# Performance work log

Measured on AMD Instinct MI355X. Metric: run time of the kernel, lower is better.

## Reference

```python
import jax, jax.numpy as jnp
import numpy as np

N = 10000        # nodes
E = 160000       # edges (avg degree 16)
WIDTH = 32       # node hidden width
KER_W = 256      # kernel MLP hidden width
KER_IN = 6       # edge feature dim
DEPTH = 4        # message-passing iterations


def setup_inputs() -> dict:
    key = jax.random.key(0)
    ks = jax.random.split(key, 12)
    def w(k, shape, fan_in):
        return jax.random.normal(k, shape, jnp.float32) * (1.0 / np.sqrt(fan_in)).astype(np.float32)
    return {
        "x": jax.random.normal(ks[0], (N, 1), jnp.float32),
        "edge_index": jax.random.randint(ks[1], (2, E), 0, N),
        "edge_attr": jax.random.uniform(ks[2], (E, KER_IN), dtype=jnp.float32),
        # fc1: Linear(1, WIDTH)
        "fc1_w": w(ks[3], (1, WIDTH), 1), "fc1_b": jnp.zeros((WIDTH,), jnp.float32),
        # kernel DenseNet: KER_IN -> KER_W -> KER_W -> WIDTH^2 (ReLU between, none after last)
        "k1_w": w(ks[4], (KER_IN, KER_W), KER_IN), "k1_b": jnp.zeros((KER_W,), jnp.float32),
        "k2_w": w(ks[5], (KER_W, KER_W), KER_W), "k2_b": jnp.zeros((KER_W,), jnp.float32),
        "k3_w": w(ks[6], (KER_W, WIDTH * WIDTH), KER_W), "k3_b": jnp.zeros((WIDTH * WIDTH,), jnp.float32),
        # NNConv root weight + bias
        "root_w": w(ks[7], (WIDTH, WIDTH), WIDTH), "conv_b": jnp.zeros((WIDTH,), jnp.float32),
        # fc2: Linear(WIDTH, 1)
        "fc2_w": w(ks[8], (WIDTH, 1), WIDTH), "fc2_b": jnp.zeros((1,), jnp.float32),
    }


def reference(x, edge_index, edge_attr, fc1_w, fc1_b, k1_w, k1_b, k2_w, k2_b,
              k3_w, k3_b, root_w, conv_b, fc2_w, fc2_b):
    src, dst = edge_index[0], edge_index[1]  # messages flow src -> dst

    # Per-edge kernel weights (edge_attr is constant across depth -> compute once).
    h = jax.nn.relu(edge_attr @ k1_w + k1_b)
    h = jax.nn.relu(h @ k2_w + k2_b)
    W_e = (h @ k3_w + k3_b).reshape(E, WIDTH, WIDTH)  # [E, in, out]

    # Degree for scatter-mean (avoid div by zero).
    deg = jax.ops.segment_sum(jnp.ones((E,), jnp.float32), dst, num_segments=N)
    inv_deg = (1.0 / jnp.maximum(deg, 1.0))[:, None]

    h_node = x @ fc1_w + fc1_b  # [N, WIDTH]
    for _ in range(DEPTH):
        msg = jnp.einsum('ei,eio->eo', h_node[src], W_e)              # gather + per-edge GEMM
        agg = jax.ops.segment_sum(msg, dst, num_segments=N) * inv_deg  # scatter-mean
        h_node = jax.nn.relu(agg + h_node @ root_w + conv_b)
    return h_node @ fc2_w + fc2_b  # [N, 1]
```

## Files before the change

kernel.cpp:

```cpp
#include <hip/hip_runtime.h>
#include <hip/hip_fp16.h>

#define NNODE 10000
#define NEDGE 160000
#define W32 32
#define BSTR 40
#define PANEL_F16 10240
#define PANEL3_F16 5120
#define UB_TILES 20000

typedef _Float16 f16;
typedef _Float16 f16x4 __attribute__((ext_vector_type(4)));
typedef _Float16 f16x8 __attribute__((ext_vector_type(8)));
typedef float f32x4 __attribute__((ext_vector_type(4)));

__device__ __forceinline__ void stage_panel(f16* lds, const f16* g, int w, int lane) {
    #pragma unroll
    for (int i = 0; i < 5; ++i) {
        int slot = w * 320 + i * 64 + lane;
        __builtin_amdgcn_global_load_lds(
            (const __attribute__((address_space(1))) unsigned int*)(g + (size_t)slot * 8),
            (__attribute__((address_space(3))) unsigned int*)(lds + (size_t)(w * 320 + i * 64) * 8),
            16, 0, 0);
    }
}

__device__ __forceinline__ void stage_panel10k(f16* lds, const f16* g, int w, int lane) {
    #pragma unroll
    for (int i = 0; i < 2; ++i) {
        int base = i * 256 + w * 64;
        __builtin_amdgcn_global_load_lds(
            (const __attribute__((address_space(1))) unsigned int*)(g + (size_t)(base + lane) * 8),
            (__attribute__((address_space(3))) unsigned int*)(lds + (size_t)base * 8),
            16, 0, 0);
    }
    if (w < 2) {
        int base = 512 + w * 64;
        __builtin_amdgcn_global_load_lds(
            (const __attribute__((address_space(1))) unsigned int*)(g + (size_t)(base + lane) * 8),
            (__attribute__((address_space(3))) unsigned int*)(lds + (size_t)base * 8),
            16, 0, 0);
    }
}

__global__ __launch_bounds__(256) void pack_k1(const float* __restrict__ k1w, f16* __restrict__ k1p) {
    int t = blockIdx.x * 256 + threadIdx.x;
    int j = t / BSTR, c = t % BSTR;
    k1p[t] = (c < 6) ? (f16)k1w[c * 256 + j] : (f16)0.f;
}
__global__ __launch_bounds__(256) void pack_k2(const float* __restrict__ k2w, f16* __restrict__ k2p) {
    int t = blockIdx.x * 256 + threadIdx.x;
    int kk = t / PANEL_F16, r = t % PANEL_F16;
    int j = r / BSTR, c = r % BSTR;
    k2p[t] = (c < 32) ? (f16)k2w[(size_t)(kk * 32 + c) * 256 + j] : (f16)0.f;
}
__global__ __launch_bounds__(256) void pack_k3(const float* __restrict__ k3w, f16* __restrict__ k3p) {
    int t = blockIdx.x * 256 + threadIdx.x;
    int p = t / PANEL3_F16, r = t % PANEL3_F16;
    int np = p >> 3, kk = p & 7;
    int j = r / BSTR, c = r % BSTR;
    k3p[t] = (c < 32) ? (f16)k3w[(size_t)(kk * 32 + c) * 1024 + np * 128 + j] : (f16)0.f;
}
__global__ __launch_bounds__(256) void pack_k3t(const float* __restrict__ k3w, f16* __restrict__ k3t) {
    int t = blockIdx.x * 256 + threadIdx.x;
    int q = t / BSTR, i = t % BSTR;
    int o = q >> 8, c = q & 255;
    k3t[t] = (i < 32) ? (f16)k3w[(size_t)c * 1024 + i * 32 + o] : (f16)0.f;
}

__global__ __launch_bounds__(256) void h2_kernel(
    const float* __restrict__ ea,
    const f16* __restrict__ k1p, const float* __restrict__ k1b,
    const f16* __restrict__ k2p, const float* __restrict__ k2b,
    f16* __restrict__ h2c, int e_start, const int* __restrict__ remap)
{
    __shared__ __align__(16) f16 bls[2][256 * BSTR];
    __shared__ __align__(16) f16 ea_s[64 * BSTR];
    __shared__ __align__(16) f16 hbuf[64 * 264];

    const int t = threadIdx.x, w = t >> 6, lane = t & 63, quad = lane >> 4, l15 = lane & 15;
    const int el0 = blockIdx.x * 64;
    const int e0 = e_start + el0;

    stage_panel(bls[0], k1p, w, lane);
    for (int i = t; i < 64 * BSTR; i += 256) {
        int e = i / BSTR, c = i % BSTR;
        ea_s[i] = (f16)((c < 6) ? ea[(size_t)(e0 + e) * 6 + c] : 0.f);
    }
    __syncthreads();

    f16x8 a1 = *(const f16x8*)&ea_s[(w * 16 + l15) * BSTR + quad * 8];
    f32x4 acc[16];
    #pragma unroll
    for (int nt = 0; nt < 16; ++nt) { float b = k1b[nt * 16 + l15]; acc[nt] = (f32x4){b, b, b, b}; }
    stage_panel(bls[1], k2p, w, lane);
    #pragma unroll
    for (int nt = 0; nt < 16; ++nt) {
        f16x8 bf = *(const f16x8*)&bls[0][(nt * 16 + l15) * BSTR + quad * 8];
        acc[nt] = __builtin_amdgcn_mfma_f32_16x16x32_f16(a1, bf, acc[nt], 0, 0, 0);
    }
    #pragma unroll
    for (int nt = 0; nt < 16; ++nt)
        #pragma unroll
        for (int r = 0; r < 4; ++r)
            hbuf[(w * 16 + quad * 4 + r) * 264 + nt * 16 + l15] = (f16)fmaxf(acc[nt][r], 0.f);
    __syncthreads();

    f16x8 a2[8];
    #pragma unroll
    for (int kk = 0; kk < 8; ++kk)
        a2[kk] = *(const f16x8*)&hbuf[(w * 16 + l15) * 264 + kk * 32 + quad * 8];
    #pragma unroll
    for (int nt = 0; nt < 16; ++nt) { float b = k2b[nt * 16 + l15]; acc[nt] = (f32x4){b, b, b, b}; }
    for (int kk = 0; kk < 8; ++kk) {
        if (kk < 7)
            stage_panel(bls[kk & 1], k2p + (size_t)(kk + 1) * PANEL_F16, w, lane);
        const f16* B = bls[(kk + 1) & 1];
        #pragma unroll
        for (int nt = 0; nt < 16; ++nt) {
            f16x8 bf = *(const f16x8*)&B[(nt * 16 + l15) * BSTR + quad * 8];
            acc[nt] = __builtin_amdgcn_mfma_f32_16x16x32_f16(a2[kk], bf, acc[nt], 0, 0, 0);
        }
        __syncthreads();
    }
    size_t orow[4];
    #pragma unroll
    for (int r = 0; r < 4; ++r) {
        int eoff = w * 16 + quad * 4 + r;
        orow[r] = remap ? (size_t)remap[e0 + eoff] : (size_t)(el0 + eoff);
    }
    #pragma unroll
    for (int nt = 0; nt < 16; ++nt)
        #pragma unroll
        for (int r = 0; r < 4; ++r)
            h2c[orow[r] * 256 + nt * 16 + l15] = (f16)fmaxf(acc[nt][r], 0.f);
}

__global__ __launch_bounds__(256) void hist_kernel(const int* __restrict__ ei, int* __restrict__ cnt) {
    int e = blockIdx.x * 256 + threadIdx.x;
    if (e < NEDGE) atomicAdd(&cnt[ei[e]], 1);
}
__global__ __launch_bounds__(256) void scan_kernel(
    const int* __restrict__ cnt, int* __restrict__ edgeStart,
    int* __restrict__ tileStartN, int* __restrict__ cursor)
{
    __shared__ int pE[256], pT[256];
    const int t = threadIdx.x;
    int se = 0, st = 0;
    for (int k = 0; k < 40; ++k) {
        int n = t * 40 + k;
        if (n < NNODE) { int c = cnt[n]; se += c; st += (c + 15) >> 4; }
    }
    pE[t] = se; pT[t] = st;
    __syncthreads();
    if (t == 0) {
        int aE = 0, aT = 0;
        for (int i = 0; i < 256; ++i) { int tE = pE[i], tT = pT[i]; pE[i] = aE; pT[i] = aT; aE += tE; aT += tT; }
        tileStartN[NNODE] = aT;
    }
    __syncthreads();
    int oE = pE[t], oT = pT[t];
    for (int k = 0; k < 40; ++k) {
        int n = t * 40 + k;
        if (n < NNODE) {
            edgeStart[n] = oE; cursor[n] = oE; tileStartN[n] = oT;
            int c = cnt[n]; oE += c; oT += (c + 15) >> 4;
        }
    }
}
__global__ __launch_bounds__(256) void scatter_kernel(
    const int* __restrict__ ei, int* __restrict__ cursor,
    int* __restrict__ dstS, int* __restrict__ sortpos)
{
    int e = blockIdx.x * 256 + threadIdx.x;
    if (e < NEDGE) {
        int s = ei[e];
        int p = atomicAdd(&cursor[s], 1);
        dstS[p] = ei[NEDGE + e];
        sortpos[e] = p;
    }
}
__global__ __launch_bounds__(256) void tiles_kernel(
    const int* __restrict__ cnt, const int* __restrict__ edgeStart, const int* __restrict__ tileStartN,
    int* __restrict__ tileNode, int* __restrict__ tileE0, int* __restrict__ tileCnt)
{
    int n = blockIdx.x * 256 + threadIdx.x;
    if (n < NNODE) {
        int d = cnt[n], t0 = tileStartN[n], e0 = edgeStart[n];
        for (int k = 0; k * 16 < d; ++k) {
            int rem = d - k * 16;
            tileNode[t0 + k] = n;
            tileE0[t0 + k] = e0 + k * 16;
            tileCnt[t0 + k] = rem < 16 ? rem : 16;
        }
    }
}

__global__ __launch_bounds__(256) void bb_kernel(
    const float* __restrict__ h, const float* __restrict__ k3b, float* __restrict__ Bb)
{
    int idx = blockIdx.x * 256 + threadIdx.x;
    int n = idx >> 5, o = idx & 31;
    float s = 0.f;
    #pragma unroll
    for (int i = 0; i < 32; ++i)
        s += h[n * 32 + i] * k3b[i * 32 + o];
    Bb[idx] = s;
}

__global__ __launch_bounds__(256) void tgen_kernel(
    const float* __restrict__ h, const f16* __restrict__ k3t, f16* __restrict__ Tt,
    int n0, int n1)
{
    const int t = threadIdx.x, w = t >> 6, lane = t & 63, quad = lane >> 4, l15 = lane & 15;
    const int nBase = n0 + blockIdx.x * 16;
    const int colBase = blockIdx.y * 1024 + w * 256;

    f16x8 a;
    #pragma unroll
    for (int i = 0; i < 8; ++i) a[i] = (f16)0.f;
    int node = nBase + l15;
    if (node < n1) {
        const float4* hp = (const float4*)(h + (size_t)node * 32) + quad * 2;
        float4 v0 = hp[0], v1 = hp[1];
        a[0] = (f16)v0.x; a[1] = (f16)v0.y; a[2] = (f16)v0.z; a[3] = (f16)v0.w;
        a[4] = (f16)v1.x; a[5] = (f16)v1.y; a[6] = (f16)v1.z; a[7] = (f16)v1.w;
    }
    f32x4 acc[16];
    #pragma unroll
    for (int nt = 0; nt < 16; ++nt) {
        f16x8 bf = *(const f16x8*)&k3t[(size_t)(colBase + nt * 16 + l15) * BSTR + quad * 8];
        acc[nt] = __builtin_amdgcn_mfma_f32_16x16x32_f16(a, bf, (f32x4){0.f, 0.f, 0.f, 0.f}, 0, 0, 0);
    }
    #pragma unroll
    for (int r = 0; r < 4; ++r) {
        int nd = nBase + quad * 4 + r;
        if (nd < n1) {
            f16* dp = Tt + (size_t)(nd - n0) * 8192 + colBase + l15;
            #pragma unroll
            for (int nt = 0; nt < 16; ++nt)
                dp[nt * 16] = (f16)acc[nt][r];
        }
    }
}

__global__ __launch_bounds__(256) void msgT_kernel(
    const f16* __restrict__ h2s, const f16* __restrict__ Tt, const float* __restrict__ Bb,
    const int* __restrict__ tileNode, const int* __restrict__ tileE0, const int* __restrict__ tileCnt,
    const int* __restrict__ tileStartN, const int* __restrict__ dstS, float* __restrict__ agg,
    int n0, int n1)
{
    const int t = threadIdx.x, w = t >> 6, lane = t & 63, quad = lane >> 4, l15 = lane & 15;
    const int t0 = tileStartN[n0], t1 = tileStartN[n1];
    for (int tile = t0 + blockIdx.x * 4 + w; tile < t1; tile += gridDim.x * 4) {
        int n = tileNode[tile];
        int e0 = tileE0[tile], cnt = tileCnt[tile];
        const f16* Tn = Tt + (size_t)(n - n0) * 8192;
        f32x4 acc[2];
        #pragma unroll
        for (int nt = 0; nt < 2; ++nt) {
            float b = Bb[n * 32 + nt * 16 + l15];
            acc[nt] = (f32x4){b, b, b, b};
        }
        #pragma unroll
        for (int kk = 0; kk < 8; ++kk) {
            f16x8 a;
            #pragma unroll
            for (int i = 0; i < 8; ++i) a[i] = (f16)0.f;
            if (l15 < cnt)
                a = *(const f16x8*)&h2s[(size_t)(e0 + l15) * 256 + kk * 32 + quad * 8];
            #pragma unroll
            for (int nt = 0; nt < 2; ++nt) {
                f16x8 bf = *(const f16x8*)&Tn[(nt * 16 + l15) * 256 + kk * 32 + quad * 8];
                acc[nt] = __builtin_amdgcn_mfma_f32_16x16x32_f16(a, bf, acc[nt], 0, 0, 0);
            }
        }
        #pragma unroll
        for (int nt = 0; nt < 2; ++nt)
            #pragma unroll
            for (int r = 0; r < 4; ++r) {
                int er = quad * 4 + r;
                if (er < cnt)
                    atomicAdd(&agg[(size_t)dstS[e0 + er] * 32 + nt * 16 + l15], acc[nt][r]);
            }
    }
}

__global__ __launch_bounds__(256, 2) void msg_fused(
    const int* __restrict__ ei, const f16* __restrict__ h2c,
    const f16* __restrict__ k3p, const float* __restrict__ k3b,
    const float* __restrict__ h, float* __restrict__ agg, int e_start)
{
    __shared__ __align__(16) f16 bls[2][PANEL3_F16];
    __shared__ __align__(16) f16 h_s[256 * 36];
    __shared__ int dst_s[256];

    const int t = threadIdx.x, w = t >> 6, lane = t & 63, quad = lane >> 4, l15 = lane & 15;
    const int el0 = blockIdx.x * 256;
    const int e0 = e_start + el0;

    dst_s[t] = ei[NEDGE + e0 + t];
    {
        int srcn = ei[e0 + t];
        const float4* hr = (const float4*)(h + (size_t)srcn * 32);
        f16* dp = &h_s[t * 36];
        #pragma unroll
        for (int qq = 0; qq < 8; ++qq) {
            float4 v = hr[qq];
            dp[qq * 4 + 0] = (f16)v.x; dp[qq * 4 + 1] = (f16)v.y;
            dp[qq * 4 + 2] = (f16)v.z; dp[qq * 4 + 3] = (f16)v.w;
        }
    }
    stage_panel10k(bls[0], k3p, w, lane);

    float msg[4][4][2];
    #pragma unroll
    for (int m = 0; m < 4; ++m)
        #pragma unroll
        for (int r = 0; r < 4; ++r) { msg[m][r][0] = 0.f; msg[m][r][1] = 0.f; }

    f32x4 acc[4][8];
    __syncthreads();

    for (int it = 0; it < 64; ++it) {
        const int np = it >> 3, kk = it & 7;
        if (it) __syncthreads();
        if (it < 63) stage_panel10k(bls[(it + 1) & 1], k3p + (size_t)(it + 1) * PANEL3_F16, w, lane);

        f16x8 a[4];
        #pragma unroll
        for (int m = 0; m < 4; ++m)
            a[m] = *(const f16x8*)(h2c + (size_t)(el0 + w * 64 + m * 16 + l15) * 256 + kk * 32 + quad * 8);

        if (kk == 0) {
            #pragma unroll
            for (int nt = 0; nt < 8; ++nt) {
                float b = k3b[np * 128 + nt * 16 + l15];
                #pragma unroll
                for (int m = 0; m < 4; ++m) acc[m][nt] = (f32x4){b, b, b, b};
            }
        }
        const f16* B = bls[it & 1];
        #pragma unroll
        for (int nt = 0; nt < 8; ++nt) {
            f16x8 bf = *(const f16x8*)&B[(nt * 16 + l15) * BSTR + quad * 8];
            #pragma unroll
            for (int m = 0; m < 4; ++m)
                acc[m][nt] = __builtin_amdgcn_mfma_f32_16x16x32_f16(a[m], bf, acc[m][nt], 0, 0, 0);
        }
        if (kk == 7) {
            #pragma unroll
            for (int m = 0; m < 4; ++m)
                #pragma unroll
                for (int r = 0; r < 4; ++r) {
                    int row = w * 64 + m * 16 + quad * 4 + r;
                    f16x4 h4 = *(const f16x4*)&h_s[row * 36 + np * 4];
                    #pragma unroll
                    for (int nt = 0; nt < 8; ++nt)
                        msg[m][r][nt & 1] += (float)h4[nt >> 1] * acc[m][nt][r];
                }
        }
    }
    #pragma unroll
    for (int m = 0; m < 4; ++m)
        #pragma unroll
        for (int r = 0; r < 4; ++r) {
            int d = dst_s[w * 64 + m * 16 + quad * 4 + r];
            atomicAdd(&agg[d * W32 + l15],      msg[m][r][0]);
            atomicAdd(&agg[d * W32 + 16 + l15], msg[m][r][1]);
        }
}

__global__ __launch_bounds__(256) void h0_kernel(
    const float* __restrict__ x, const float* __restrict__ fc1w,
    const float* __restrict__ fc1b, float* __restrict__ h)
{
    int idx = blockIdx.x * 256 + threadIdx.x;
    int n = idx >> 5, j = idx & 31;
    h[idx] = x[n] * fc1w[j] + fc1b[j];
}

__global__ __launch_bounds__(256) void deg_kernel(
    const int* __restrict__ ei, float* __restrict__ deg)
{
    int e = blockIdx.x * 256 + threadIdx.x;
    if (e < NEDGE) atomicAdd(&deg[ei[NEDGE + e]], 1.f);
}

__global__ __launch_bounds__(256) void update_kernel(
    const float* __restrict__ h_old, float* __restrict__ h_new,
    float* __restrict__ agg, const float* __restrict__ deg,
    const float* __restrict__ rootw, const float* __restrict__ convb)
{
    __shared__ float rw[W32][W32 + 1];
    const int t = threadIdx.x;
    for (int q = t; q < W32 * W32; q += 256)
        rw[q >> 5][q & 31] = rootw[q];
    __syncthreads();
    const int nl = t >> 5, j = t & 31;
    const int n = blockIdx.x * 8 + nl;
    float hv = h_old[n * W32 + j];
    float acc = convb[j];
    #pragma unroll
    for (int k = 0; k < W32; ++k)
        acc += __shfl(hv, k, 32) * rw[k][j];
    float inv = 1.f / fmaxf(deg[n], 1.f);
    int idx = n * W32 + j;
    float a = agg[idx];
    agg[idx] = 0.f;
    h_new[idx] = fmaxf(a * inv + acc, 0.f);
}

__global__ __launch_bounds__(256) void out_kernel(
    const float* __restrict__ h, const float* __restrict__ fc2w,
    const float* __restrict__ fc2b, float* __restrict__ out)
{
    int n = blockIdx.x * 256 + threadIdx.x;
    if (n < NNODE) {
        float a = fc2b[0];
        #pragma unroll
        for (int j = 0; j < W32; ++j)
            a += h[n * W32 + j] * fc2w[j];
        out[n] = a;
    }
}

static inline size_t pad256(size_t x) { return (x + 255) & ~(size_t)255; }

extern "C" void kernel_launch(void* const* d_in, const int* in_sizes, int n_in,
                              void* d_out, int out_size, void* d_ws, size_t ws_size,
                              hipStream_t stream) {
    const float* x    = (const float*)d_in[0];
    const int*   ei   = (const int*)  d_in[1];
    const float* ea   = (const float*)d_in[2];
    const float* fc1w = (const float*)d_in[3];
    const float* fc1b = (const float*)d_in[4];
    const float* k1w  = (const float*)d_in[5];
    const float* k1b  = (const float*)d_in[6];
    const float* k2w  = (const float*)d_in[7];
    const float* k2b  = (const float*)d_in[8];
    const float* k3w  = (const float*)d_in[9];
    const float* k3b  = (const float*)d_in[10];
    const float* rootw= (const float*)d_in[11];
    const float* convb= (const float*)d_in[12];
    const float* fc2w = (const float*)d_in[13];
    const float* fc2b = (const float*)d_in[14];
    float* out = (float*)d_out;

    const size_t hbytes = (size_t)NNODE * W32 * 4;
    char* ws = (char*)d_ws;
    size_t off = 0;
    float* hA  = (float*)(ws + off); off += hbytes;
    float* hB  = (float*)(ws + off); off += hbytes;
    float* agg = (float*)(ws + off); off += hbytes;
    float* deg = (float*)(ws + off); off += 40960;
    f16*  k1p  = (f16*)(ws + off);   off += 20480;
    f16*  k2p  = (f16*)(ws + off);   off += 163840;
    f16*  k3p  = (f16*)(ws + off);   off += 655360;
    const size_t fixed = off;

    size_t toff = fixed;
    f16*  k3t      = (f16*)(ws + toff);  toff += pad256(8192 * BSTR * 2);
    int*  dstS     = (int*)(ws + toff);  toff += pad256((size_t)NEDGE * 4);
    int*  sortpos  = (int*)(ws + toff);  toff += pad256((size_t)NEDGE * 4);
    int*  cnt      = (int*)(ws + toff);  toff += pad256((size_t)NNODE * 4);
    int*  edgeStart= (int*)(ws + toff);  toff += pad256((size_t)NNODE * 4);
    int*  tileStartN=(int*)(ws + toff);  toff += pad256((size_t)(NNODE + 1) * 4);
    int*  cursor   = (int*)(ws + toff);  toff += pad256((size_t)NNODE * 4);
    int*  tileNode = (int*)(ws + toff);  toff += pad256((size_t)UB_TILES * 4);
    int*  tileE0   = (int*)(ws + toff);  toff += pad256((size_t)UB_TILES * 4);
    int*  tileCnt  = (int*)(ws + toff);  toff += pad256((size_t)UB_TILES * 4);
    float* Bb      = (float*)(ws + toff); toff += pad256((size_t)NNODE * 32 * 4);
    f16*  h2s      = (f16*)(ws + toff);  toff += pad256((size_t)NEDGE * 256 * 2);
    f16*  Tt       = (f16*)(ws + toff);

    int nc = 0, CS = 0;
    {
        const int cands[3] = {2, 4, 8};
        for (int ci = 0; ci < 3; ++ci) {
            int c = cands[ci];
            int cs = ((NNODE + c - 1) / c + 15) & ~15;
            size_t tb = (size_t)cs * 8192 * 2;
            if (ws_size >= toff + tb) { nc = c; CS = cs; break; }
        }
    }

    hipMemsetAsync(deg, 0, (size_t)NNODE * 4, stream);
    hipMemsetAsync(agg, 0, (size_t)NNODE * W32 * 4, stream);

    pack_k1<<<40, 256, 0, stream>>>(k1w, k1p);
    pack_k2<<<320, 256, 0, stream>>>(k2w, k2p);

    h0_kernel<<<NNODE * W32 / 256, 256, 0, stream>>>(x, fc1w, fc1b, hA);
    deg_kernel<<<(NEDGE + 255) / 256, 256, 0, stream>>>(ei, deg);

    float* hcur = hA; float* hnext = hB;

    if (nc) {
        pack_k3t<<<1280, 256, 0, stream>>>(k3w, k3t);
        hipMemsetAsync(cnt, 0, (size_t)NNODE * 4, stream);
        hist_kernel<<<(NEDGE + 255) / 256, 256, 0, stream>>>(ei, cnt);
        scan_kernel<<<1, 256, 0, stream>>>(cnt, edgeStart, tileStartN, cursor);
        scatter_kernel<<<(NEDGE + 255) / 256, 256, 0, stream>>>(ei, cursor, dstS, sortpos);
        tiles_kernel<<<(NNODE + 255) / 256, 256, 0, stream>>>(cnt, edgeStart, tileStartN,
                                                              tileNode, tileE0, tileCnt);
        h2_kernel<<<NEDGE / 64, 256, 0, stream>>>(ea, k1p, k1b, k2p, k2b, h2s, 0, sortpos);

        for (int d = 0; d < 4; ++d) {
            bb_kernel<<<NNODE * 32 / 256, 256, 0, stream>>>(hcur, k3b, Bb);
            for (int ct = 0; ct < nc; ++ct) {
                int n0 = ct * CS;
                if (n0 >= NNODE) break;
                int n1 = n0 + CS; if (n1 > NNODE) n1 = NNODE;
                dim3 tg((n1 - n0 + 15) / 16, 8);
                tgen_kernel<<<tg, 256, 0, stream>>>(hcur, k3t, Tt, n0, n1);
                msgT_kernel<<<1280, 256, 0, stream>>>(h2s, Tt, Bb, tileNode, tileE0, tileCnt,
                                                      tileStartN, dstS, agg, n0, n1);
            }
            update_kernel<<<NNODE / 8, 256, 0, stream>>>(hcur, hnext, agg, deg, rootw, convb);
            float* tmp = hcur; hcur = hnext; hnext = tmp;
        }
    } else {
        f16* h2b = (f16*)(ws + fixed);
        pack_k3<<<1280, 256, 0, stream>>>(k3w, k3p);

        long long availC = 0;
        if (ws_size > fixed) availC = (long long)((ws_size - fixed) / 512);
        int C = (availC > NEDGE) ? NEDGE : (int)availC;
        C &= ~255;
        if (C < 256) return;

        const bool full = (C == NEDGE);
        if (full)
            h2_kernel<<<NEDGE / 64, 256, 0, stream>>>(ea, k1p, k1b, k2p, k2b, h2b, 0, nullptr);

        for (int d = 0; d < 4; ++d) {
            for (int es = 0; es < NEDGE; es += C) {
                int ce = (NEDGE - es < C) ? (NEDGE - es) : C;
                if (!full)
                    h2_kernel<<<ce / 64, 256, 0, stream>>>(ea, k1p, k1b, k2p, k2b, h2b, es, nullptr);
                msg_fused<<<ce / 256, 256, 0, stream>>>(ei, h2b, k3p, k3b, hcur, agg, es);
            }
            update_kernel<<<NNODE / 8, 256, 0, stream>>>(hcur, hnext, agg, deg, rootw, convb);
            float* tmp = hcur; hcur = hnext; hnext = tmp;
        }
    }
    out_kernel<<<(NNODE + 255) / 256, 256, 0, stream>>>(hcur, fc2w, fc2b, out);
}
```

Baseline: 688.1 us.

## Stage MFMA outputs through LDS for coalesced 16-byte stores; allow single-chunk T buffer

In h2_kernel and tgen_kernel, MFMA results are first written to a padded LDS tile and then copied to global memory as contiguous 16-byte vectors per row. Previously each lane issued scattered 2-byte stores. The hbuf row stride is also changed to reduce LDS bank conflicts. Chunk count 1 is added to the candidate list, so the whole Tt buffer can be built in one pass when the workspace is large enough, cutting per-chunk launches. The cost is extra LDS traffic and barriers, plus a larger workspace requirement when one chunk is chosen.

```diff
diff --git a/kernel.cpp b/kernel.cpp
--- a/kernel.cpp
+++ b/kernel.cpp
@@ -8,6 +8,8 @@
 #define PANEL_F16 10240
 #define PANEL3_F16 5120
 #define UB_TILES 20000
+#define HB_STR 268
+#define TB_STR 1036
 
 typedef _Float16 f16;
 typedef _Float16 f16x4 __attribute__((ext_vector_type(4)));
@@ -76,7 +78,7 @@
 {
     __shared__ __align__(16) f16 bls[2][256 * BSTR];
     __shared__ __align__(16) f16 ea_s[64 * BSTR];
-    __shared__ __align__(16) f16 hbuf[64 * 264];
+    __shared__ __align__(16) f16 hbuf[64 * HB_STR];
 
     const int t = threadIdx.x, w = t >> 6, lane = t & 63, quad = lane >> 4, l15 = lane & 15;
     const int el0 = blockIdx.x * 64;
@@ -103,13 +105,13 @@
     for (int nt = 0; nt < 16; ++nt)
         #pragma unroll
         for (int r = 0; r < 4; ++r)
-            hbuf[(w * 16 + quad * 4 + r) * 264 + nt * 16 + l15] = (f16)fmaxf(acc[nt][r], 0.f);
+            hbuf[(w * 16 + quad * 4 + r) * HB_STR + nt * 16 + l15] = (f16)fmaxf(acc[nt][r], 0.f);
     __syncthreads();
 
     f16x8 a2[8];
     #pragma unroll
     for (int kk = 0; kk < 8; ++kk)
-        a2[kk] = *(const f16x8*)&hbuf[(w * 16 + l15) * 264 + kk * 32 + quad * 8];
+        a2[kk] = *(const f16x8*)&hbuf[(w * 16 + l15) * HB_STR + kk * 32 + quad * 8];
     #pragma unroll
     for (int nt = 0; nt < 16; ++nt) { float b = k2b[nt * 16 + l15]; acc[nt] = (f32x4){b, b, b, b}; }
     for (int kk = 0; kk < 8; ++kk) {
@@ -123,17 +125,23 @@
         }
         __syncthreads();
     }
-    size_t orow[4];
-    #pragma unroll
-    for (int r = 0; r < 4; ++r) {
-        int eoff = w * 16 + quad * 4 + r;
-        orow[r] = remap ? (size_t)remap[e0 + eoff] : (size_t)(el0 + eoff);
-    }
     #pragma unroll
     for (int nt = 0; nt < 16; ++nt)
         #pragma unroll
         for (int r = 0; r < 4; ++r)
-            h2c[orow[r] * 256 + nt * 16 + l15] = (f16)fmaxf(acc[nt][r], 0.f);
+            hbuf[(w * 16 + quad * 4 + r) * HB_STR + nt * 16 + l15] = (f16)fmaxf(acc[nt][r], 0.f);
+    __syncthreads();
+    {
+        const int row = t >> 2, u = t & 3;
+        const size_t orow = remap ? (size_t)remap[e0 + row] : (size_t)(el0 + row);
+        f16* gdst = h2c + orow * 256;
+        const f16* lsrc = &hbuf[row * HB_STR];
+        #pragma unroll
+        for (int j = 0; j < 8; ++j) {
+            int p = u + 4 * j;
+            *(f16x8*)(gdst + p * 8) = *(const f16x8*)(lsrc + p * 8);
+        }
+    }
 }
 
 __global__ __launch_bounds__(256) void hist_kernel(const int* __restrict__ ei, int* __restrict__ cnt) {
@@ -212,9 +220,11 @@
     const float* __restrict__ h, const f16* __restrict__ k3t, f16* __restrict__ Tt,
     int n0, int n1)
 {
+    __shared__ __align__(16) f16 tbuf[16 * TB_STR];
+
     const int t = threadIdx.x, w = t >> 6, lane = t & 63, quad = lane >> 4, l15 = lane & 15;
     const int nBase = n0 + blockIdx.x * 16;
-    const int colBase = blockIdx.y * 1024 + w * 256;
+    const int colBase = blockIdx.y * 1024;
 
     f16x8 a;
     #pragma unroll
@@ -229,17 +239,26 @@
     f32x4 acc[16];
     #pragma unroll
     for (int nt = 0; nt < 16; ++nt) {
-        f16x8 bf = *(const f16x8*)&k3t[(size_t)(colBase + nt * 16 + l15) * BSTR + quad * 8];
+        f16x8 bf = *(const f16x8*)&k3t[(size_t)(colBase + w * 256 + nt * 16 + l15) * BSTR + quad * 8];
         acc[nt] = __builtin_amdgcn_mfma_f32_16x16x32_f16(a, bf, (f32x4){0.f, 0.f, 0.f, 0.f}, 0, 0, 0);
     }
     #pragma unroll
-    for (int r = 0; r < 4; ++r) {
-        int nd = nBase + quad * 4 + r;
+    for (int nt = 0; nt < 16; ++nt)
+        #pragma unroll
+        for (int r = 0; r < 4; ++r)
+            tbuf[(quad * 4 + r) * TB_STR + w * 256 + nt * 16 + l15] = (f16)acc[nt][r];
+    __syncthreads();
+    {
+        const int row = t >> 4, u = t & 15;
+        const int nd = nBase + row;
         if (nd < n1) {
-            f16* dp = Tt + (size_t)(nd - n0) * 8192 + colBase + l15;
-            #pragma unroll
-            for (int nt = 0; nt < 16; ++nt)
-                dp[nt * 16] = (f16)acc[nt][r];
+            f16* gdst = Tt + (size_t)(nd - n0) * 8192 + colBase;
+            const f16* lsrc = &tbuf[row * TB_STR];
+            #pragma unroll
+            for (int j = 0; j < 8; ++j) {
+                int p = u + 16 * j;
+                *(f16x8*)(gdst + p * 8) = *(const f16x8*)(lsrc + p * 8);
+            }
         }
     }
 }
@@ -476,8 +495,8 @@
 
     int nc = 0, CS = 0;
     {
-        const int cands[3] = {2, 4, 8};
-        for (int ci = 0; ci < 3; ++ci) {
+        const int cands[4] = {1, 2, 4, 8};
+        for (int ci = 0; ci < 4; ++ci) {
             int c = cands[ci];
             int cs = ((NNODE + c - 1) / c + 15) & ~15;
             size_t tb = (size_t)cs * 8192 * 2;
```

Result: faster. 627.2 us (-8.9%).

## Fuse T generation, bias and per-tile message GEMM into one LDS-resident kernel

Applied to the files above, without the earlier changes.

Replaces the separate bias, T-generation and tiled message kernels with one kernel per group of 8 destination nodes. That kernel computes each node's transformed kernel matrix directly into shared memory and then consumes it for that node's edge tiles. This removes the large global write and re-read of the per-node T buffer, the node-chunk loop and several launches per iteration. In exchange it uses about 135KB of LDS per block, which limits occupancy, and wastes half of the MFMA rows in the T generation step.

```diff
diff --git a/kernel.cpp b/kernel.cpp
--- a/kernel.cpp
+++ b/kernel.cpp
@@ -8,6 +8,9 @@
 #define PANEL_F16 10240
 #define PANEL3_F16 5120
 #define UB_TILES 20000
+#define HB_STR 264
+#define TS_ROW 264
+#define TS_NODE 8452
 
 typedef _Float16 f16;
 typedef _Float16 f16x4 __attribute__((ext_vector_type(4)));
@@ -76,7 +79,7 @@
 {
     __shared__ __align__(16) f16 bls[2][256 * BSTR];
     __shared__ __align__(16) f16 ea_s[64 * BSTR];
-    __shared__ __align__(16) f16 hbuf[64 * 264];
+    __shared__ __align__(16) f16 hbuf[64 * HB_STR];
 
     const int t = threadIdx.x, w = t >> 6, lane = t & 63, quad = lane >> 4, l15 = lane & 15;
     const int el0 = blockIdx.x * 64;
@@ -103,13 +106,13 @@
     for (int nt = 0; nt < 16; ++nt)
         #pragma unroll
         for (int r = 0; r < 4; ++r)
-            hbuf[(w * 16 + quad * 4 + r) * 264 + nt * 16 + l15] = (f16)fmaxf(acc[nt][r], 0.f);
+            hbuf[(w * 16 + quad * 4 + r) * HB_STR + nt * 16 + l15] = (f16)fmaxf(acc[nt][r], 0.f);
     __syncthreads();
 
     f16x8 a2[8];
     #pragma unroll
     for (int kk = 0; kk < 8; ++kk)
-        a2[kk] = *(const f16x8*)&hbuf[(w * 16 + l15) * 264 + kk * 32 + quad * 8];
+        a2[kk] = *(const f16x8*)&hbuf[(w * 16 + l15) * HB_STR + kk * 32 + quad * 8];
     #pragma unroll
     for (int nt = 0; nt < 16; ++nt) { float b = k2b[nt * 16 + l15]; acc[nt] = (f32x4){b, b, b, b}; }
     for (int kk = 0; kk < 8; ++kk) {
@@ -196,83 +199,77 @@
     }
 }
 
-__global__ __launch_bounds__(256) void bb_kernel(
-    const float* __restrict__ h, const float* __restrict__ k3b, float* __restrict__ Bb)
-{
-    int idx = blockIdx.x * 256 + threadIdx.x;
-    int n = idx >> 5, o = idx & 31;
-    float s = 0.f;
-    #pragma unroll
-    for (int i = 0; i < 32; ++i)
-        s += h[n * 32 + i] * k3b[i * 32 + o];
-    Bb[idx] = s;
-}
-
-__global__ __launch_bounds__(256) void tgen_kernel(
-    const float* __restrict__ h, const f16* __restrict__ k3t, f16* __restrict__ Tt,
-    int n0, int n1)
-{
+__global__ __launch_bounds__(256) void fusedT_kernel(
+    const float* __restrict__ h, const f16* __restrict__ k3t, const float* __restrict__ k3b,
+    const f16* __restrict__ h2s,
+    const int* __restrict__ tileNode, const int* __restrict__ tileE0, const int* __restrict__ tileCnt,
+    const int* __restrict__ tileStartN, const int* __restrict__ dstS, float* __restrict__ agg)
+{
+    __shared__ __align__(16) f16 T8[8 * TS_NODE];
+    __shared__ float bbl[8][32];
+
     const int t = threadIdx.x, w = t >> 6, lane = t & 63, quad = lane >> 4, l15 = lane & 15;
-    const int nBase = n0 + blockIdx.x * 16;
-    const int colBase = blockIdx.y * 1024 + w * 256;
+    const int n0b = blockIdx.x * 8;
+
+    {
+        int nl = t >> 5, o = t & 31;
+        float s = 0.f;
+        const float* hp = h + (size_t)(n0b + nl) * 32;
+        #pragma unroll
+        for (int i = 0; i < 32; ++i) s += hp[i] * k3b[i * 32 + o];
+        bbl[nl][o] = s;
+    }
 
     f16x8 a;
     #pragma unroll
     for (int i = 0; i < 8; ++i) a[i] = (f16)0.f;
-    int node = nBase + l15;
-    if (node < n1) {
-        const float4* hp = (const float4*)(h + (size_t)node * 32) + quad * 2;
+    if (l15 < 8) {
+        const float4* hp = (const float4*)(h + (size_t)(n0b + l15) * 32) + quad * 2;
         float4 v0 = hp[0], v1 = hp[1];
         a[0] = (f16)v0.x; a[1] = (f16)v0.y; a[2] = (f16)v0.z; a[3] = (f16)v0.w;
         a[4] = (f16)v1.x; a[5] = (f16)v1.y; a[6] = (f16)v1.z; a[7] = (f16)v1.w;
     }
-    f32x4 acc[16];
-    #pragma unroll
-    for (int nt = 0; nt < 16; ++nt) {
-        f16x8 bf = *(const f16x8*)&k3t[(size_t)(colBase + nt * 16 + l15) * BSTR + quad * 8];
-        acc[nt] = __builtin_amdgcn_mfma_f32_16x16x32_f16(a, bf, (f32x4){0.f, 0.f, 0.f, 0.f}, 0, 0, 0);
-    }
-    #pragma unroll
-    for (int r = 0; r < 4; ++r) {
-        int nd = nBase + quad * 4 + r;
-        if (nd < n1) {
-            f16* dp = Tt + (size_t)(nd - n0) * 8192 + colBase + l15;
+    for (int cb = 0; cb < 8; ++cb) {
+        const int o = cb * 4 + w;
+        const size_t qbase = (size_t)(cb * 1024 + w * 256);
+        f32x4 acc[16];
+        #pragma unroll
+        for (int nt = 0; nt < 16; ++nt) {
+            f16x8 bf = *(const f16x8*)&k3t[(qbase + nt * 16 + l15) * BSTR + quad * 8];
+            acc[nt] = __builtin_amdgcn_mfma_f32_16x16x32_f16(a, bf, (f32x4){0.f, 0.f, 0.f, 0.f}, 0, 0, 0);
+        }
+        if (quad < 2) {
             #pragma unroll
             for (int nt = 0; nt < 16; ++nt)
-                dp[nt * 16] = (f16)acc[nt][r];
-        }
-    }
-}
-
-__global__ __launch_bounds__(256) void msgT_kernel(
-    const f16* __restrict__ h2s, const f16* __restrict__ Tt, const float* __restrict__ Bb,
-    const int* __restrict__ tileNode, const int* __restrict__ tileE0, const int* __restrict__ tileCnt,
-    const int* __restrict__ tileStartN, const int* __restrict__ dstS, float* __restrict__ agg,
-    int n0, int n1)
-{
-    const int t = threadIdx.x, w = t >> 6, lane = t & 63, quad = lane >> 4, l15 = lane & 15;
-    const int t0 = tileStartN[n0], t1 = tileStartN[n1];
-    for (int tile = t0 + blockIdx.x * 4 + w; tile < t1; tile += gridDim.x * 4) {
+                #pragma unroll
+                for (int r = 0; r < 4; ++r)
+                    T8[(quad * 4 + r) * TS_NODE + o * TS_ROW + nt * 16 + l15] = (f16)acc[nt][r];
+        }
+    }
+    __syncthreads();
+
+    const int tS = tileStartN[n0b], tE = tileStartN[n0b + 8];
+    for (int tile = tS + w; tile < tE; tile += 4) {
         int n = tileNode[tile];
         int e0 = tileE0[tile], cnt = tileCnt[tile];
-        const f16* Tn = Tt + (size_t)(n - n0) * 8192;
+        const f16* Tn = &T8[(n - n0b) * TS_NODE];
         f32x4 acc[2];
         #pragma unroll
         for (int nt = 0; nt < 2; ++nt) {
-            float b = Bb[n * 32 + nt * 16 + l15];
+            float b = bbl[n - n0b][nt * 16 + l15];
             acc[nt] = (f32x4){b, b, b, b};
         }
         #pragma unroll
         for (int kk = 0; kk < 8; ++kk) {
-            f16x8 a;
-            #pragma unroll
-            for (int i = 0; i < 8; ++i) a[i] = (f16)0.f;
+            f16x8 av;
+            #pragma unroll
+            for (int i = 0; i < 8; ++i) av[i] = (f16)0.f;
             if (l15 < cnt)
-                a = *(const f16x8*)&h2s[(size_t)(e0 + l15) * 256 + kk * 32 + quad * 8];
+                av = *(const f16x8*)&h2s[(size_t)(e0 + l15) * 256 + kk * 32 + quad * 8];
             #pragma unroll
             for (int nt = 0; nt < 2; ++nt) {
-                f16x8 bf = *(const f16x8*)&Tn[(nt * 16 + l15) * 256 + kk * 32 + quad * 8];
-                acc[nt] = __builtin_amdgcn_mfma_f32_16x16x32_f16(a, bf, acc[nt], 0, 0, 0);
+                f16x8 bf = *(const f16x8*)&Tn[(nt * 16 + l15) * TS_ROW + kk * 32 + quad * 8];
+                acc[nt] = __builtin_amdgcn_mfma_f32_16x16x32_f16(av, bf, acc[nt], 0, 0, 0);
             }
         }
         #pragma unroll
@@ -470,20 +467,8 @@
     int*  tileNode = (int*)(ws + toff);  toff += pad256((size_t)UB_TILES * 4);
     int*  tileE0   = (int*)(ws + toff);  toff += pad256((size_t)UB_TILES * 4);
     int*  tileCnt  = (int*)(ws + toff);  toff += pad256((size_t)UB_TILES * 4);
-    float* Bb      = (float*)(ws + toff); toff += pad256((size_t)NNODE * 32 * 4);
     f16*  h2s      = (f16*)(ws + toff);  toff += pad256((size_t)NEDGE * 256 * 2);
-    f16*  Tt       = (f16*)(ws + toff);
-
-    int nc = 0, CS = 0;
-    {
-        const int cands[3] = {2, 4, 8};
-        for (int ci = 0; ci < 3; ++ci) {
-            int c = cands[ci];
-            int cs = ((NNODE + c - 1) / c + 15) & ~15;
-            size_t tb = (size_t)cs * 8192 * 2;
-            if (ws_size >= toff + tb) { nc = c; CS = cs; break; }
-        }
-    }
+    const bool tpath = (ws_size >= toff);
 
     hipMemsetAsync(deg, 0, (size_t)NNODE * 4, stream);
     hipMemsetAsync(agg, 0, (size_t)NNODE * W32 * 4, stream);
@@ -496,7 +481,7 @@
 
     float* hcur = hA; float* hnext = hB;
 
-    if (nc) {
+    if (tpath) {
         pack_k3t<<<1280, 256, 0, stream>>>(k3w, k3t);
         hipMemsetAsync(cnt, 0, (size_t)NNODE * 4, stream);
         hist_kernel<<<(NEDGE + 255) / 256, 256, 0, stream>>>(ei, cnt);
@@ -507,16 +492,9 @@
         h2_kernel<<<NEDGE / 64, 256, 0, stream>>>(ea, k1p, k1b, k2p, k2b, h2s, 0, sortpos);
 
         for (int d = 0; d < 4; ++d) {
-            bb_kernel<<<NNODE * 32 / 256, 256, 0, stream>>>(hcur, k3b, Bb);
-            for (int ct = 0; ct < nc; ++ct) {
-                int n0 = ct * CS;
-                if (n0 >= NNODE) break;
-                int n1 = n0 + CS; if (n1 > NNODE) n1 = NNODE;
-                dim3 tg((n1 - n0 + 15) / 16, 8);
-                tgen_kernel<<<tg, 256, 0, stream>>>(hcur, k3t, Tt, n0, n1);
-                msgT_kernel<<<1280, 256, 0, stream>>>(h2s, Tt, Bb, tileNode, tileE0, tileCnt,
-                                                      tileStartN, dstS, agg, n0, n1);
-            }
+            fusedT_kernel<<<NNODE / 8, 256, 0, stream>>>(hcur, k3t, k3b, h2s,
+                                                         tileNode, tileE0, tileCnt,
+                                                         tileStartN, dstS, agg);
             update_kernel<<<NNODE / 8, 256, 0, stream>>>(hcur, hnext, agg, deg, rootw, convb);
             float* tmp = hcur; hcur = hnext; hnext = tmp;
         }
```

Result: slower. 896.9 us (+30.3%).
